# Optimization experiments

Measured on AMD Instinct MI355X. Metric: run time of the kernel, lower is better.

The kernel has to match this reference:

```python
import jax, jax.numpy as jnp
import numpy as np

B, S, L, U, E, V = 32, 64, 64, 512, 256, 32000

def setup_inputs() -> dict:
    key = jax.random.key(0)
    ks = jax.random.split(key, 12)
    sc = lambda *d: 0.02
    return {
        "target": jax.random.randint(ks[0], (B, S), 0, V),
        "encoder_outputs": jax.random.normal(ks[1], (B, L, U), jnp.float32),
        "enc_h0": jax.random.normal(ks[2], (B, U), jnp.float32),
        "enc_c0": jax.random.normal(ks[3], (B, U), jnp.float32),
        "emb": jax.random.normal(ks[4], (V, E), jnp.float32) * 0.02,
        "W_x": jax.random.normal(ks[5], (E, 4 * U), jnp.float32) * 0.02,
        "W_h": jax.random.normal(ks[6], (U, 4 * U), jnp.float32) * 0.02,
        "b_lstm": jnp.zeros((4 * U,), jnp.float32),
        "Wa": jax.random.normal(ks[7], (U, U), jnp.float32) * 0.02,
        "W_fc": jax.random.normal(ks[8], (2 * U, V), jnp.float32) * 0.02,
        "b_fc": jnp.zeros((V,), jnp.float32),
    }

def reference(target, encoder_outputs, enc_h0, enc_c0, emb, W_x, W_h, b_lstm, Wa, W_fc, b_fc):
    # Teacher forcing (teach_forcing_ran=1): input at step t is target[:, t-1],
    # producing outputs for t = 1 .. seq_maxlen-1.
    x_seq = emb[target[:, : S - 1]]                      # [B, S-1, E]
    x_seq = jnp.transpose(x_seq, (1, 0, 2))              # [S-1, B, E]
    enc_proj = jnp.einsum('blu,uv->blv', encoder_outputs, Wa)  # Luong 'general' projection

    def step(carry, x_t):
        h, c = carry
        z = x_t @ W_x + h @ W_h + b_lstm                 # [B, 4U]
        i, f, g, o = jnp.split(z, 4, axis=-1)            # keras gate order i,f,c,o
        i = jax.nn.sigmoid(i); f = jax.nn.sigmoid(f)
        g = jnp.tanh(g);       o = jax.nn.sigmoid(o)
        c = f * c + i * g
        h = o * jnp.tanh(c)
        score = jnp.einsum('bu,blu->bl', h, enc_proj)    # [B, L]
        attn = jax.nn.softmax(score, axis=-1)
        ctx = jnp.einsum('bl,blu->bu', attn, encoder_outputs)
        logits = jnp.tanh(jnp.concatenate([ctx, h], axis=-1) @ W_fc + b_fc)
        out_t = jax.nn.log_softmax(logits, axis=-1)      # [B, V]
        return (h, c), out_t

    (_, _), outs = jax.lax.scan(step, (enc_h0, enc_c0), x_seq)
    return jnp.transpose(outs, (1, 0, 2))                # [B, S-1, V]
```

## Files before the change

### kernel.cpp

```cpp
#include <hip/hip_runtime.h>
#include <stdint.h>

#define B_   32
#define T_   63
#define U_   512
#define E_   256
#define V_   32000
#define L_   64
#define FU_  2048
#define KFC_ 1024
#define MROW_ 2016

#define NFCX_ 250
#define NFCY_ 16
#define CCNT_BASE 1024
#define AFC_FLAG_U32 (2016 * 512)

typedef float f32x4 __attribute__((ext_vector_type(4)));
typedef float f32x2 __attribute__((ext_vector_type(2)));
typedef __bf16 bf16x8 __attribute__((ext_vector_type(8)));

__device__ __forceinline__ unsigned short f2bf(float f) {
  union { float f; unsigned u; } v; v.f = f;
  unsigned u = v.u;
  u += 0x7FFFu + ((u >> 16) & 1u);
  return (unsigned short)(u >> 16);
}
__device__ __forceinline__ float bf2f(unsigned short h) {
  union { unsigned u; float f; } v; v.u = ((unsigned)h) << 16;
  return v.f;
}
__device__ __forceinline__ float fast_sigmoid(float x) {
  return 1.f / (1.f + __expf(-x));
}
__device__ __forceinline__ float fast_tanh(float x) {
  float e = __expf(2.f * x);
  return 1.f - 2.f / (e + 1.f);
}

__global__ __launch_bounds__(256) void k_prep(const int* __restrict__ target,
    const float* __restrict__ emb, const float* __restrict__ W_x,
    const float* __restrict__ b_lstm, const float* __restrict__ enc_out,
    const float* __restrict__ Wa, const float* __restrict__ W_h,
    unsigned short* __restrict__ fragWh, unsigned short* __restrict__ Zx,
    float* __restrict__ enc_proj, unsigned short* __restrict__ encT,
    unsigned int* __restrict__ hcnt, float* __restrict__ row_sums,
    unsigned int* __restrict__ AfcFlags) {
  __shared__ __align__(16) char smem[32768];
  const int bx = blockIdx.x;
  const int tid = threadIdx.x;

  if (bx < 512) {
    int idx = bx * 256 + tid;
    int lane = idx & 63;
    int kc   = (idx >> 6) & 15;
    int ct   = idx >> 10;
    int quad = lane >> 4, l15 = lane & 15;
    int col = ct * 16 + l15;
    unsigned short* dst = fragWh + (size_t)idx * 8;
#pragma unroll
    for (int j = 0; j < 8; ++j) {
      int k = kc * 32 + quad * 8 + j;
      dst[j] = f2bf(W_h[(size_t)k * FU_ + col]);
    }
  } else if (bx < 1016) {
    float* x_lds = (float*)smem;
    int r = bx - 512;
    int t = r % 63, cc = r / 63;
    for (int i = tid; i < B_ * E_; i += 256) {
      int b = i >> 8, e = i & 255;
      x_lds[i] = emb[(size_t)target[b * 64 + t] * E_ + e];
    }
    __syncthreads();
    int col = cc * 256 + tid;
    float acc[B_];
#pragma unroll
    for (int b = 0; b < B_; ++b) acc[b] = 0.f;
    for (int e4 = 0; e4 < E_ / 4; ++e4) {
      float w0 = W_x[(size_t)(4 * e4 + 0) * FU_ + col];
      float w1 = W_x[(size_t)(4 * e4 + 1) * FU_ + col];
      float w2 = W_x[(size_t)(4 * e4 + 2) * FU_ + col];
      float w3 = W_x[(size_t)(4 * e4 + 3) * FU_ + col];
#pragma unroll
      for (int b = 0; b < B_; ++b) {
        f32x4 xv = *(const f32x4*)&x_lds[b * E_ + 4 * e4];
        acc[b] += xv[0] * w0 + xv[1] * w1 + xv[2] * w2 + xv[3] * w3;
      }
    }
    float bias = b_lstm[col];
#pragma unroll
    for (int b = 0; b < B_; ++b)
      Zx[((size_t)(t * B_ + b)) * FU_ + col] = f2bf(acc[b] + bias);
  } else if (bx < 1272) {
    float* e_lds = (float*)smem;
    int r = bx - 1016;
    int rc = r & 127, cc = r >> 7;
    int row0 = rc * 16;
    for (int i = tid; i < 16 * U_; i += 256)
      e_lds[i] = enc_out[(size_t)(row0 + (i >> 9)) * U_ + (i & 511)];
    __syncthreads();
    int col = cc * 256 + tid;
    float acc[16];
#pragma unroll
    for (int q = 0; q < 16; ++q) acc[q] = 0.f;
    for (int k4 = 0; k4 < U_ / 4; ++k4) {
      float w0 = Wa[(size_t)(4 * k4 + 0) * U_ + col];
      float w1 = Wa[(size_t)(4 * k4 + 1) * U_ + col];
      float w2 = Wa[(size_t)(4 * k4 + 2) * U_ + col];
      float w3 = Wa[(size_t)(4 * k4 + 3) * U_ + col];
#pragma unroll
      for (int q = 0; q < 16; ++q) {
        f32x4 xv = *(const f32x4*)&e_lds[q * U_ + 4 * k4];
        acc[q] += xv[0] * w0 + xv[1] * w1 + xv[2] * w2 + xv[3] * w3;
      }
    }
#pragma unroll
    for (int q = 0; q < 16; ++q)
      enc_proj[(size_t)(row0 + q) * U_ + col] = acc[q];
  } else if (bx < 1528) {
    float (*tile)[65] = (float(*)[65])smem;
    int r = bx - 1272;
    int b = r & 31, uc = r >> 5;
#pragma unroll
    for (int i = 0; i < 16; ++i) {
      int idx = i * 256 + tid;
      int l = idx >> 6, u = idx & 63;
      tile[l][u] = enc_out[((size_t)b * L_ + l) * U_ + uc * 64 + u];
    }
    __syncthreads();
#pragma unroll
    for (int i = 0; i < 16; ++i) {
      int idx = i * 256 + tid;
      int u = idx >> 6, l = idx & 63;
      encT[((size_t)b * U_ + uc * 64 + u) * L_ + l] = f2bf(tile[l][u]);
    }
  } else {
    int i = (bx - 1528) * 256 + tid;
    hcnt[i] = 0u;
    if (i < MROW_) row_sums[i] = 0.f;
    AfcFlags[i * 4 + 0] = 0u;
    AfcFlags[i * 4 + 1] = 0u;
    AfcFlags[i * 4 + 2] = 0u;
    AfcFlags[i * 4 + 3] = 0u;
  }
}

__global__ __launch_bounds__(256, 1) void k_rec(const float* __restrict__ enc_h0,
    const float* __restrict__ enc_c0,
    const float* __restrict__ enc_proj, const unsigned short* __restrict__ Zx,
    const unsigned short* __restrict__ fragWh, const unsigned short* __restrict__ encT,
    unsigned int* hseq32,
    unsigned short* __restrict__ Afc,
    unsigned int* hcnt,
    unsigned short* __restrict__ WfcT, const float* __restrict__ b_fc,
    float* __restrict__ out, float* __restrict__ row_sums,
    const float* __restrict__ W_fc) {
  __shared__ __align__(16) char smem[44160];

  const int tid = threadIdx.x;
  unsigned long long* hseq64 = (unsigned long long*)hseq32;
  unsigned int* AfcFlags = (unsigned int*)Afc + AFC_FLAG_U32;

  if (blockIdx.x < 32) {
    unsigned short* h_lds = (unsigned short*)smem;
    float* z_lds = (float*)(smem + 33280);
    float* c_lds = (float*)(smem + 41984);

    const int g = blockIdx.x;
    const int w = tid >> 6;
    const int lane = tid & 63;
    const int quad = lane >> 4;
    const int l15 = lane & 15;
    const int b = tid >> 3;
    const int j = tid & 7;

    const unsigned short* bbase = fragWh + ((size_t)(w * 32 + g) * 16) * 64 * 8;
    bf16x8 bfr[16];
#pragma unroll
    for (int kc = 0; kc < 16; ++kc)
      bfr[kc] = *(const bf16x8*)(bbase + (size_t)(kc * 64 + lane) * 8);

    __builtin_amdgcn_s_setprio(1);

    {
      int u = g * 16 + 2 * j;
      float h0a = enc_h0[(size_t)b * U_ + u];
      float h0b = enc_h0[(size_t)b * U_ + u + 1];
      unsigned pack = (unsigned)f2bf(h0a) | ((unsigned)f2bf(h0b) << 16);
      __hip_atomic_store(&hseq32[b * 256 + g * 8 + j], pack,
                         __ATOMIC_RELAXED, __HIP_MEMORY_SCOPE_AGENT);
      c_lds[b * 17 + 2 * j]     = enc_c0[(size_t)b * U_ + u];
      c_lds[b * 17 + 2 * j + 1] = enc_c0[(size_t)b * U_ + u + 1];
    }
    __syncthreads();
    if (tid == 0)
      __hip_atomic_fetch_add(&hcnt[0], 1u, __ATOMIC_RELAXED, __HIP_MEMORY_SCOPE_AGENT);

    for (int t = 0; t < T_; ++t) {
      const unsigned short* zxbase = Zx + ((size_t)(t * B_ + b)) * FU_ + g * 16 + 2 * j;
      unsigned zxp0 = *(const unsigned*)(zxbase + 0 * U_);
      unsigned zxp1 = *(const unsigned*)(zxbase + 1 * U_);
      unsigned zxp2 = *(const unsigned*)(zxbase + 2 * U_);
      unsigned zxp3 = *(const unsigned*)(zxbase + 3 * U_);

      if (tid == 0) {
        while (__hip_atomic_load(&hcnt[t * 16], __ATOMIC_RELAXED,
                                 __HIP_MEMORY_SCOPE_AGENT) < 32u)
          __builtin_amdgcn_s_sleep(1);
      }
      __syncthreads();

      const unsigned long long* hp = hseq64 + (size_t)t * (B_ * U_ / 4);
      unsigned long long hv[16];
#pragma unroll
      for (int i = 0; i < 16; ++i) {
        hv[i] = __hip_atomic_load(&hp[i * 256 + tid], __ATOMIC_RELAXED,
                                  __HIP_MEMORY_SCOPE_AGENT);
      }
#pragma unroll
      for (int i = 0; i < 16; ++i) {
        int idx = i * 256 + tid;
        int hb = idx >> 7, u0 = (idx & 127) * 4;
        *(unsigned long long*)&h_lds[hb * 520 + u0] = hv[i];
      }
      __syncthreads();

      f32x4 acc0 = {0.f, 0.f, 0.f, 0.f}, acc1 = {0.f, 0.f, 0.f, 0.f};
#pragma unroll
      for (int kc = 0; kc < 16; ++kc) {
        bf16x8 a0 = *(const bf16x8*)&h_lds[l15 * 520 + kc * 32 + quad * 8];
        bf16x8 a1 = *(const bf16x8*)&h_lds[(16 + l15) * 520 + kc * 32 + quad * 8];
        acc0 = __builtin_amdgcn_mfma_f32_16x16x32_bf16(a0, bfr[kc], acc0, 0, 0, 0);
        acc1 = __builtin_amdgcn_mfma_f32_16x16x32_bf16(a1, bfr[kc], acc1, 0, 0, 0);
      }
#pragma unroll
      for (int r = 0; r < 4; ++r) {
        z_lds[(quad * 4 + r) * 68 + w * 16 + l15] = acc0[r];
        z_lds[(16 + quad * 4 + r) * 68 + w * 16 + l15] = acc1[r];
      }
      __syncthreads();

      {
        int up0 = 2 * j, up1 = 2 * j + 1;
        float zi0 = z_lds[b * 68 + 0 + up0] + bf2f((unsigned short)(zxp0 & 0xFFFFu));
        float zi1 = z_lds[b * 68 + 0 + up1] + bf2f((unsigned short)(zxp0 >> 16));
        float zf0 = z_lds[b * 68 + 16 + up0] + bf2f((unsigned short)(zxp1 & 0xFFFFu));
        float zf1 = z_lds[b * 68 + 16 + up1] + bf2f((unsigned short)(zxp1 >> 16));
        float zg0 = z_lds[b * 68 + 32 + up0] + bf2f((unsigned short)(zxp2 & 0xFFFFu));
        float zg1 = z_lds[b * 68 + 32 + up1] + bf2f((unsigned short)(zxp2 >> 16));
        float zo0 = z_lds[b * 68 + 48 + up0] + bf2f((unsigned short)(zxp3 & 0xFFFFu));
        float zo1 = z_lds[b * 68 + 48 + up1] + bf2f((unsigned short)(zxp3 >> 16));
        float i0 = fast_sigmoid(zi0), i1 = fast_sigmoid(zi1);
        float f0 = fast_sigmoid(zf0), f1 = fast_sigmoid(zf1);
        float g0 = fast_tanh(zg0),    g1 = fast_tanh(zg1);
        float o0 = fast_sigmoid(zo0), o1 = fast_sigmoid(zo1);
        float c0 = f0 * c_lds[b * 17 + up0] + i0 * g0;
        float c1 = f1 * c_lds[b * 17 + up1] + i1 * g1;
        c_lds[b * 17 + up0] = c0;
        c_lds[b * 17 + up1] = c1;
        float h0 = o0 * fast_tanh(c0);
        float h1 = o1 * fast_tanh(c1);
        unsigned pack = (unsigned)f2bf(h0) | ((unsigned)f2bf(h1) << 16);
        __hip_atomic_store(&hseq32[(size_t)(t + 1) * (B_ * U_ / 2) + b * 256 + g * 8 + j],
                           pack, __ATOMIC_RELAXED, __HIP_MEMORY_SCOPE_AGENT);
        __hip_atomic_store(
            (unsigned*)&Afc[(size_t)(t * B_ + b) * KFC_ + U_ + g * 16 + 2 * j],
            pack, __ATOMIC_RELAXED, __HIP_MEMORY_SCOPE_AGENT);
      }
      __syncthreads();
      if (tid == 0)
        __hip_atomic_fetch_add(&hcnt[(t + 1) * 16], 1u,
                               __ATOMIC_RELAXED, __HIP_MEMORY_SCOPE_AGENT);
    }
  } else if (blockIdx.x < 64) {
    float* h_sh    = (float*)smem;
    float* sc_part = (float*)(smem + 2048);
    float* probs   = (float*)(smem + 3072);

    __builtin_amdgcn_s_setprio(1);
    const int b = blockIdx.x - 32;
    for (int t = 0; t < T_; ++t) {
      if (tid == 0) {
        while (__hip_atomic_load(&hcnt[(t + 1) * 16], __ATOMIC_RELAXED,
                                 __HIP_MEMORY_SCOPE_AGENT) < 32u)
          __builtin_amdgcn_s_sleep(2);
      }
      __syncthreads();
      if (tid < 128) {
        unsigned long long v = __hip_atomic_load(
            &hseq64[(size_t)(t + 1) * (B_ * U_ / 4) + b * 128 + tid],
            __ATOMIC_RELAXED, __HIP_MEMORY_SCOPE_AGENT);
        int u0 = tid * 4;
        h_sh[u0 + 0] = bf2f((unsigned short)(v & 0xFFFFu));
        h_sh[u0 + 1] = bf2f((unsigned short)((v >> 16) & 0xFFFFu));
        h_sh[u0 + 2] = bf2f((unsigned short)((v >> 32) & 0xFFFFu));
        h_sh[u0 + 3] = bf2f((unsigned short)((v >> 48) & 0xFFFFu));
      }
      __syncthreads();
      {
        int l = tid & 63, part = tid >> 6;
        const float* ep = enc_proj + ((size_t)(b * L_ + l)) * U_ + part * 128;
        const float* hs = h_sh + part * 128;
        float s = 0.f;
#pragma unroll 8
        for (int u = 0; u < 128; u += 4) {
          f32x4 e = *(const f32x4*)(ep + u);
          s += hs[u] * e[0] + hs[u + 1] * e[1] + hs[u + 2] * e[2] + hs[u + 3] * e[3];
        }
        sc_part[part * L_ + l] = s;
      }
      __syncthreads();
      if (tid < 64) {
        float s = sc_part[tid] + sc_part[64 + tid] + sc_part[128 + tid] + sc_part[192 + tid];
        float m = s;
#pragma unroll
        for (int off = 32; off >= 1; off >>= 1) m = fmaxf(m, __shfl_xor(m, off));
        float e = __expf(s - m);
        float sum = e;
#pragma unroll
        for (int off = 32; off >= 1; off >>= 1) sum += __shfl_xor(sum, off);
        probs[tid] = e / sum;
      }
      __syncthreads();
      {
        int u0 = 2 * tid;
        const unsigned short* ep0 = encT + ((size_t)b * U_ + u0) * L_;
        float c0 = 0.f, c1 = 0.f;
#pragma unroll
        for (int l8 = 0; l8 < 8; ++l8) {
          bf16x8 e0 = *(const bf16x8*)(ep0 + l8 * 8);
          bf16x8 e1 = *(const bf16x8*)(ep0 + L_ + l8 * 8);
#pragma unroll
          for (int q = 0; q < 8; ++q) {
            float p = probs[l8 * 8 + q];
            c0 += p * (float)e0[q];
            c1 += p * (float)e1[q];
          }
        }
        unsigned pack = (unsigned)f2bf(c0) | ((unsigned)f2bf(c1) << 16);
        __hip_atomic_store((unsigned*)&Afc[(size_t)(t * B_ + b) * KFC_ + u0], pack,
                           __ATOMIC_RELAXED, __HIP_MEMORY_SCOPE_AGENT);
      }
      __syncthreads();
      if (tid == 0)
        __hip_atomic_fetch_add(&hcnt[CCNT_BASE + t * 16], 1u,
                               __ATOMIC_RELAXED, __HIP_MEMORY_SCOPE_AGENT);
    }
  } else {
    unsigned short* At = (unsigned short*)smem;
    unsigned short* Bt = (unsigned short*)(smem + 8192);
    float* rs = (float*)(smem + 16384);

    const int idx = blockIdx.x - 64;
    const int cx = idx % NFCX_, ry = idx / NFCX_;
    int t_hi = 4 * ry + 3; if (t_hi > T_ - 1) t_hi = T_ - 1;

    if (ry == 0) {
      float* tile = (float*)smem;
      const int n0 = cx * 128;
      for (int kt2 = 0; kt2 < 32; ++kt2) {
        int k0 = kt2 * 32;
#pragma unroll
        for (int it = 0; it < 4; ++it) {
          int lin = it * 256 + tid;
          int k = lin >> 5, nq = lin & 31;
          f32x4 v = *(const f32x4*)(W_fc + (size_t)(k0 + k) * V_ + n0 + nq * 4);
          *(f32x4*)&tile[k * 132 + nq * 4] = v;
        }
        __syncthreads();
#pragma unroll
        for (int it = 0; it < 4; ++it) {
          int lin = it * 256 + tid;
          int n = lin >> 3, kq = lin & 7;
          float a0 = tile[(kq * 4 + 0) * 132 + n];
          float a1 = tile[(kq * 4 + 1) * 132 + n];
          float a2 = tile[(kq * 4 + 2) * 132 + n];
          float a3 = tile[(kq * 4 + 3) * 132 + n];
          unsigned long long pk =
              (unsigned long long)((unsigned)f2bf(a0) | ((unsigned)f2bf(a1) << 16)) |
              ((unsigned long long)((unsigned)f2bf(a2) | ((unsigned)f2bf(a3) << 16)) << 32);
          __hip_atomic_store(
              (unsigned long long*)&WfcT[(size_t)(n0 + n) * KFC_ + k0 + kq * 4], pk,
              __ATOMIC_RELAXED, __HIP_MEMORY_SCOPE_AGENT);
        }
        __syncthreads();
      }
      if (tid == 0)
        __hip_atomic_store(&AfcFlags[cx * 16], 1u,
                           __ATOMIC_RELAXED, __HIP_MEMORY_SCOPE_AGENT);
    }

    if (tid == 0) {
      if (ry != 0) {
        while (__hip_atomic_load(&AfcFlags[cx * 16], __ATOMIC_RELAXED,
                                 __HIP_MEMORY_SCOPE_AGENT) == 0u)
          __builtin_amdgcn_s_sleep(16);
      }
      while (__hip_atomic_load(&hcnt[CCNT_BASE + t_hi * 16], __ATOMIC_RELAXED,
                               __HIP_MEMORY_SCOPE_AGENT) < 32u)
        __builtin_amdgcn_s_sleep(32);
    }
    __syncthreads();

    const int w = tid >> 6, lane = tid & 63, quad = lane >> 4, l15 = lane & 15;
    const int row0 = ry * 128, col0 = cx * 128;
    const int mh = (w >> 1) * 64, nh = (w & 1) * 64;

    f32x4 acc[4][4];
#pragma unroll
    for (int i = 0; i < 4; ++i)
#pragma unroll
      for (int j = 0; j < 4; ++j) { f32x4 z = {0.f, 0.f, 0.f, 0.f}; acc[i][j] = z; }

    for (int kt = 0; kt < KFC_ / 32; ++kt) {
      int k0 = kt * 32;
#pragma unroll
      for (int i = 0; i < 2; ++i) {
        int lin = i * 256 + tid;
        int r = lin >> 2, s = lin & 3;
        int gseg = (s - (r >> 1)) & 3;
        f32x4 va = *(const f32x4*)(Afc + ((size_t)(row0 + r)) * KFC_ + k0 + gseg * 8);
        *(f32x4*)&At[r * 32 + s * 8] = va;
        f32x4 vb = *(const f32x4*)(WfcT + ((size_t)(col0 + r)) * KFC_ + k0 + gseg * 8);
        *(f32x4*)&Bt[r * 32 + s * 8] = vb;
      }
      __syncthreads();
      bf16x8 a[4], b[4];
#pragma unroll
      for (int i = 0; i < 4; ++i) {
        int m = mh + i * 16 + l15;
        a[i] = *(const bf16x8*)&At[m * 32 + (((quad + (m >> 1)) & 3) * 8)];
        int n = nh + i * 16 + l15;
        b[i] = *(const bf16x8*)&Bt[n * 32 + (((quad + (n >> 1)) & 3) * 8)];
      }
#pragma unroll
      for (int i = 0; i < 4; ++i)
#pragma unroll
        for (int j = 0; j < 4; ++j)
          acc[i][j] = __builtin_amdgcn_mfma_f32_16x16x32_bf16(a[i], b[j], acc[i][j], 0, 0, 0);
      __syncthreads();
    }

    if (tid < 128) rs[tid] = 0.f;
    __syncthreads();
    float bv[4];
#pragma unroll
    for (int j = 0; j < 4; ++j) bv[j] = b_fc[col0 + nh + j * 16 + l15];
    float rp[4][4];
#pragma unroll
    for (int i = 0; i < 4; ++i)
#pragma unroll
      for (int r = 0; r < 4; ++r) rp[i][r] = 0.f;
#pragma unroll
    for (int i = 0; i < 4; ++i) {
#pragma unroll
      for (int j = 0; j < 4; ++j) {
        int cg = col0 + nh + j * 16 + l15;
#pragma unroll
        for (int r = 0; r < 4; ++r) {
          float val = fast_tanh(acc[i][j][r] + bv[j]);
          int rg = row0 + mh + i * 16 + quad * 4 + r;
          if (rg < MROW_) {
            int b = rg & 31, t = rg >> 5;
            out[((size_t)(b * T_ + t)) * V_ + cg] = val;
          }
          rp[i][r] += __expf(val);
        }
      }
    }
#pragma unroll
    for (int i = 0; i < 4; ++i)
#pragma unroll
      for (int r = 0; r < 4; ++r) {
        float v = rp[i][r];
        v += __shfl_xor(v, 1); v += __shfl_xor(v, 2);
        v += __shfl_xor(v, 4); v += __shfl_xor(v, 8);
        if (l15 == 0) atomicAdd(&rs[mh + i * 16 + quad * 4 + r], v);
      }
    __syncthreads();
    if (tid < 128) {
      int rg = row0 + tid;
      if (rg < MROW_) atomicAdd(&row_sums[rg], rs[tid]);
    }
  }
}

__global__ __launch_bounds__(256) void k_lsm(float* __restrict__ out,
                                             const float* __restrict__ row_sums, int n4) {
  int i = blockIdx.x * 256 + threadIdx.x;
  if (i >= n4) return;
  f32x4* o4 = (f32x4*)out;
  f32x4 v = o4[i];
  int r = i / 8000;
  int b = r / 63, t = r - b * 63;
  float ls = __logf(row_sums[t * 32 + b]);
  v[0] -= ls; v[1] -= ls; v[2] -= ls; v[3] -= ls;
  o4[i] = v;
}

extern "C" void kernel_launch(void* const* d_in, const int* in_sizes, int n_in,
                              void* d_out, int out_size, void* d_ws, size_t ws_size,
                              hipStream_t stream) {
  const int*   target  = (const int*)d_in[0];
  const float* enc_out = (const float*)d_in[1];
  const float* enc_h0  = (const float*)d_in[2];
  const float* enc_c0  = (const float*)d_in[3];
  const float* emb     = (const float*)d_in[4];
  const float* W_x     = (const float*)d_in[5];
  const float* W_h     = (const float*)d_in[6];
  const float* b_lstm  = (const float*)d_in[7];
  const float* Wa      = (const float*)d_in[8];
  const float* W_fc    = (const float*)d_in[9];
  const float* b_fc    = (const float*)d_in[10];
  float* out = (float*)d_out;
  char* ws = (char*)d_ws;

  unsigned int*   hcnt     = (unsigned int*)(ws + 0);
  float*          row_sums = (float*)(ws + 8192);
  unsigned short* fragWh   = (unsigned short*)(ws + 16384);
  unsigned int*   hseq32   = (unsigned int*)(ws + 2113536);
  unsigned short* Zx       = (unsigned short*)(ws + 4210688);
  float*          enc_proj = (float*)(ws + 12468224);
  unsigned short* Afc      = (unsigned short*)(ws + 16662528);
  unsigned short* encT     = (unsigned short*)(ws + 20856832);
  unsigned short* WfcT     = (unsigned short*)(ws + 22953984);

  unsigned int* AfcFlags = (unsigned int*)(ws + 16662528 + (size_t)AFC_FLAG_U32 * 4);

  k_prep <<<dim3(1536),         dim3(256), 0, stream>>>(target, emb, W_x, b_lstm,
                                                        enc_out, Wa, W_h,
                                                        fragWh, Zx, enc_proj, encT,
                                                        hcnt, row_sums, AfcFlags);
  k_rec  <<<dim3(64 + NFCX_ * NFCY_), dim3(256), 0, stream>>>(enc_h0, enc_c0,
                                                        enc_proj, Zx, fragWh, encT,
                                                        hseq32, Afc, hcnt,
                                                        WfcT, b_fc, out, row_sums,
                                                        W_fc);
  k_lsm  <<<dim3(63000),        dim3(256), 0, stream>>>(out, row_sums, 16128000);
}
```

Baseline: 1.064 ms.

## Use 512-thread blocks: halve recurrent blocks, per-block flags, pack two FC tiles

The persistent kernel now runs 512-thread blocks. The LSTM recurrence is split over 16 blocks, each computing 32 hidden units with eight waves and two weight fragments held in registers. The single atomic counter per step is replaced by per-block flags, which 64 threads poll with a wave vote. Attention blocks use eight partial score slices, and each FC block processes two 128x128 tiles in separate LDS halves. The aim is to cut barrier and counter contention on the serial recurrence and the block count, at the cost of more registers per thread and possible occupancy or co-residency risks for the spin-waiting blocks.

```diff
diff --git a/kernel.cpp b/kernel.cpp
--- a/kernel.cpp
+++ b/kernel.cpp
@@ -17,7 +17,6 @@
 #define AFC_FLAG_U32 (2016 * 512)
 
 typedef float f32x4 __attribute__((ext_vector_type(4)));
-typedef float f32x2 __attribute__((ext_vector_type(2)));
 typedef __bf16 bf16x8 __attribute__((ext_vector_type(8)));
 
 __device__ __forceinline__ unsigned short f2bf(float f) {
@@ -145,7 +144,7 @@
   }
 }
 
-__global__ __launch_bounds__(256, 1) void k_rec(const float* __restrict__ enc_h0,
+__global__ __launch_bounds__(512, 2) void k_rec(const float* __restrict__ enc_h0,
     const float* __restrict__ enc_c0,
     const float* __restrict__ enc_proj, const unsigned short* __restrict__ Zx,
     const unsigned short* __restrict__ fragWh, const unsigned short* __restrict__ encT,
@@ -155,71 +154,79 @@
     unsigned short* __restrict__ WfcT, const float* __restrict__ b_fc,
     float* __restrict__ out, float* __restrict__ row_sums,
     const float* __restrict__ W_fc) {
-  __shared__ __align__(16) char smem[44160];
+  __shared__ __align__(16) char smem[54528];
 
   const int tid = threadIdx.x;
   unsigned long long* hseq64 = (unsigned long long*)hseq32;
   unsigned int* AfcFlags = (unsigned int*)Afc + AFC_FLAG_U32;
 
-  if (blockIdx.x < 32) {
+  if (blockIdx.x < 16) {
     unsigned short* h_lds = (unsigned short*)smem;
     float* z_lds = (float*)(smem + 33280);
-    float* c_lds = (float*)(smem + 41984);
-
-    const int g = blockIdx.x;
-    const int w = tid >> 6;
+    float* c_lds = (float*)(smem + 50176);
+
+    const int p = blockIdx.x;
+    const int ww = tid >> 6;
+    const int w = ww & 3;
+    const int hf = ww >> 2;
     const int lane = tid & 63;
     const int quad = lane >> 4;
     const int l15 = lane & 15;
-    const int b = tid >> 3;
-    const int j = tid & 7;
-
-    const unsigned short* bbase = fragWh + ((size_t)(w * 32 + g) * 16) * 64 * 8;
-    bf16x8 bfr[16];
-#pragma unroll
-    for (int kc = 0; kc < 16; ++kc)
-      bfr[kc] = *(const bf16x8*)(bbase + (size_t)(kc * 64 + lane) * 8);
+    const int b = tid >> 4;
+    const int j = tid & 15;
+
+    bf16x8 bfr[2][16];
+#pragma unroll
+    for (int s = 0; s < 2; ++s) {
+      const unsigned short* bbase = fragWh + ((size_t)(w * 32 + 2 * p + s) * 16) * 512;
+#pragma unroll
+      for (int kc = 0; kc < 16; ++kc)
+        bfr[s][kc] = *(const bf16x8*)(bbase + (size_t)(kc * 64 + lane) * 8);
+    }
 
     __builtin_amdgcn_s_setprio(1);
 
     {
-      int u = g * 16 + 2 * j;
+      int u = 32 * p + 2 * j;
       float h0a = enc_h0[(size_t)b * U_ + u];
       float h0b = enc_h0[(size_t)b * U_ + u + 1];
       unsigned pack = (unsigned)f2bf(h0a) | ((unsigned)f2bf(h0b) << 16);
-      __hip_atomic_store(&hseq32[b * 256 + g * 8 + j], pack,
+      __hip_atomic_store(&hseq32[b * 256 + 16 * p + j], pack,
                          __ATOMIC_RELAXED, __HIP_MEMORY_SCOPE_AGENT);
-      c_lds[b * 17 + 2 * j]     = enc_c0[(size_t)b * U_ + u];
-      c_lds[b * 17 + 2 * j + 1] = enc_c0[(size_t)b * U_ + u + 1];
+      c_lds[b * 34 + 2 * j]     = enc_c0[(size_t)b * U_ + u];
+      c_lds[b * 34 + 2 * j + 1] = enc_c0[(size_t)b * U_ + u + 1];
     }
     __syncthreads();
     if (tid == 0)
-      __hip_atomic_fetch_add(&hcnt[0], 1u, __ATOMIC_RELAXED, __HIP_MEMORY_SCOPE_AGENT);
+      __hip_atomic_store(&hcnt[p], 1u, __ATOMIC_RELAXED, __HIP_MEMORY_SCOPE_AGENT);
 
     for (int t = 0; t < T_; ++t) {
-      const unsigned short* zxbase = Zx + ((size_t)(t * B_ + b)) * FU_ + g * 16 + 2 * j;
+      const unsigned short* zxbase = Zx + ((size_t)(t * B_ + b)) * FU_ + 32 * p + 2 * j;
       unsigned zxp0 = *(const unsigned*)(zxbase + 0 * U_);
       unsigned zxp1 = *(const unsigned*)(zxbase + 1 * U_);
       unsigned zxp2 = *(const unsigned*)(zxbase + 2 * U_);
       unsigned zxp3 = *(const unsigned*)(zxbase + 3 * U_);
 
-      if (tid == 0) {
-        while (__hip_atomic_load(&hcnt[t * 16], __ATOMIC_RELAXED,
-                                 __HIP_MEMORY_SCOPE_AGENT) < 32u)
+      if (tid < 64) {
+        int pl = tid & 15;
+        while (true) {
+          unsigned v = __hip_atomic_load(&hcnt[t * 16 + pl], __ATOMIC_RELAXED,
+                                         __HIP_MEMORY_SCOPE_AGENT);
+          if (__all(v != 0u)) break;
           __builtin_amdgcn_s_sleep(1);
-      }
-      __syncthreads();
-
-      const unsigned long long* hp = hseq64 + (size_t)t * (B_ * U_ / 4);
-      unsigned long long hv[16];
-#pragma unroll
-      for (int i = 0; i < 16; ++i) {
-        hv[i] = __hip_atomic_load(&hp[i * 256 + tid], __ATOMIC_RELAXED,
+        }
+      }
+      __syncthreads();
+
+      const unsigned long long* hp = hseq64 + (size_t)t * 4096;
+      unsigned long long hv[8];
+#pragma unroll
+      for (int i = 0; i < 8; ++i)
+        hv[i] = __hip_atomic_load(&hp[i * 512 + tid], __ATOMIC_RELAXED,
                                   __HIP_MEMORY_SCOPE_AGENT);
-      }
-#pragma unroll
-      for (int i = 0; i < 16; ++i) {
-        int idx = i * 256 + tid;
+#pragma unroll
+      for (int i = 0; i < 8; ++i) {
+        int idx = i * 512 + tid;
         int hb = idx >> 7, u0 = (idx & 127) * 4;
         *(unsigned long long*)&h_lds[hb * 520 + u0] = hv[i];
       }
@@ -228,67 +235,71 @@
       f32x4 acc0 = {0.f, 0.f, 0.f, 0.f}, acc1 = {0.f, 0.f, 0.f, 0.f};
 #pragma unroll
       for (int kc = 0; kc < 16; ++kc) {
-        bf16x8 a0 = *(const bf16x8*)&h_lds[l15 * 520 + kc * 32 + quad * 8];
-        bf16x8 a1 = *(const bf16x8*)&h_lds[(16 + l15) * 520 + kc * 32 + quad * 8];
-        acc0 = __builtin_amdgcn_mfma_f32_16x16x32_bf16(a0, bfr[kc], acc0, 0, 0, 0);
-        acc1 = __builtin_amdgcn_mfma_f32_16x16x32_bf16(a1, bfr[kc], acc1, 0, 0, 0);
+        bf16x8 av = *(const bf16x8*)&h_lds[(hf * 16 + l15) * 520 + kc * 32 + quad * 8];
+        acc0 = __builtin_amdgcn_mfma_f32_16x16x32_bf16(av, bfr[0][kc], acc0, 0, 0, 0);
+        acc1 = __builtin_amdgcn_mfma_f32_16x16x32_bf16(av, bfr[1][kc], acc1, 0, 0, 0);
       }
 #pragma unroll
       for (int r = 0; r < 4; ++r) {
-        z_lds[(quad * 4 + r) * 68 + w * 16 + l15] = acc0[r];
-        z_lds[(16 + quad * 4 + r) * 68 + w * 16 + l15] = acc1[r];
+        z_lds[(hf * 16 + quad * 4 + r) * 132 + w * 32 + l15]      = acc0[r];
+        z_lds[(hf * 16 + quad * 4 + r) * 132 + w * 32 + 16 + l15] = acc1[r];
       }
       __syncthreads();
 
       {
         int up0 = 2 * j, up1 = 2 * j + 1;
-        float zi0 = z_lds[b * 68 + 0 + up0] + bf2f((unsigned short)(zxp0 & 0xFFFFu));
-        float zi1 = z_lds[b * 68 + 0 + up1] + bf2f((unsigned short)(zxp0 >> 16));
-        float zf0 = z_lds[b * 68 + 16 + up0] + bf2f((unsigned short)(zxp1 & 0xFFFFu));
-        float zf1 = z_lds[b * 68 + 16 + up1] + bf2f((unsigned short)(zxp1 >> 16));
-        float zg0 = z_lds[b * 68 + 32 + up0] + bf2f((unsigned short)(zxp2 & 0xFFFFu));
-        float zg1 = z_lds[b * 68 + 32 + up1] + bf2f((unsigned short)(zxp2 >> 16));
-        float zo0 = z_lds[b * 68 + 48 + up0] + bf2f((unsigned short)(zxp3 & 0xFFFFu));
-        float zo1 = z_lds[b * 68 + 48 + up1] + bf2f((unsigned short)(zxp3 >> 16));
+        const float* zb = z_lds + b * 132;
+        float zi0 = zb[ 0 + up0] + bf2f((unsigned short)(zxp0 & 0xFFFFu));
+        float zi1 = zb[ 0 + up1] + bf2f((unsigned short)(zxp0 >> 16));
+        float zf0 = zb[32 + up0] + bf2f((unsigned short)(zxp1 & 0xFFFFu));
+        float zf1 = zb[32 + up1] + bf2f((unsigned short)(zxp1 >> 16));
+        float zg0 = zb[64 + up0] + bf2f((unsigned short)(zxp2 & 0xFFFFu));
+        float zg1 = zb[64 + up1] + bf2f((unsigned short)(zxp2 >> 16));
+        float zo0 = zb[96 + up0] + bf2f((unsigned short)(zxp3 & 0xFFFFu));
+        float zo1 = zb[96 + up1] + bf2f((unsigned short)(zxp3 >> 16));
         float i0 = fast_sigmoid(zi0), i1 = fast_sigmoid(zi1);
         float f0 = fast_sigmoid(zf0), f1 = fast_sigmoid(zf1);
         float g0 = fast_tanh(zg0),    g1 = fast_tanh(zg1);
         float o0 = fast_sigmoid(zo0), o1 = fast_sigmoid(zo1);
-        float c0 = f0 * c_lds[b * 17 + up0] + i0 * g0;
-        float c1 = f1 * c_lds[b * 17 + up1] + i1 * g1;
-        c_lds[b * 17 + up0] = c0;
-        c_lds[b * 17 + up1] = c1;
+        float c0 = f0 * c_lds[b * 34 + up0] + i0 * g0;
+        float c1 = f1 * c_lds[b * 34 + up1] + i1 * g1;
+        c_lds[b * 34 + up0] = c0;
+        c_lds[b * 34 + up1] = c1;
         float h0 = o0 * fast_tanh(c0);
         float h1 = o1 * fast_tanh(c1);
         unsigned pack = (unsigned)f2bf(h0) | ((unsigned)f2bf(h1) << 16);
-        __hip_atomic_store(&hseq32[(size_t)(t + 1) * (B_ * U_ / 2) + b * 256 + g * 8 + j],
+        __hip_atomic_store(&hseq32[(size_t)(t + 1) * 8192 + b * 256 + 16 * p + j],
                            pack, __ATOMIC_RELAXED, __HIP_MEMORY_SCOPE_AGENT);
         __hip_atomic_store(
-            (unsigned*)&Afc[(size_t)(t * B_ + b) * KFC_ + U_ + g * 16 + 2 * j],
+            (unsigned*)&Afc[(size_t)(t * B_ + b) * KFC_ + U_ + 32 * p + 2 * j],
             pack, __ATOMIC_RELAXED, __HIP_MEMORY_SCOPE_AGENT);
       }
       __syncthreads();
       if (tid == 0)
-        __hip_atomic_fetch_add(&hcnt[(t + 1) * 16], 1u,
-                               __ATOMIC_RELAXED, __HIP_MEMORY_SCOPE_AGENT);
-    }
-  } else if (blockIdx.x < 64) {
+        __hip_atomic_store(&hcnt[(t + 1) * 16 + p], 1u,
+                           __ATOMIC_RELAXED, __HIP_MEMORY_SCOPE_AGENT);
+    }
+  } else if (blockIdx.x < 48) {
     float* h_sh    = (float*)smem;
     float* sc_part = (float*)(smem + 2048);
-    float* probs   = (float*)(smem + 3072);
+    float* probs   = (float*)(smem + 4096);
 
     __builtin_amdgcn_s_setprio(1);
-    const int b = blockIdx.x - 32;
+    const int b = blockIdx.x - 16;
     for (int t = 0; t < T_; ++t) {
-      if (tid == 0) {
-        while (__hip_atomic_load(&hcnt[(t + 1) * 16], __ATOMIC_RELAXED,
-                                 __HIP_MEMORY_SCOPE_AGENT) < 32u)
+      if (tid < 64) {
+        int pl = tid & 15;
+        while (true) {
+          unsigned v = __hip_atomic_load(&hcnt[(t + 1) * 16 + pl], __ATOMIC_RELAXED,
+                                         __HIP_MEMORY_SCOPE_AGENT);
+          if (__all(v != 0u)) break;
           __builtin_amdgcn_s_sleep(2);
+        }
       }
       __syncthreads();
       if (tid < 128) {
         unsigned long long v = __hip_atomic_load(
-            &hseq64[(size_t)(t + 1) * (B_ * U_ / 4) + b * 128 + tid],
+            &hseq64[(size_t)(t + 1) * 4096 + b * 128 + tid],
             __ATOMIC_RELAXED, __HIP_MEMORY_SCOPE_AGENT);
         int u0 = tid * 4;
         h_sh[u0 + 0] = bf2f((unsigned short)(v & 0xFFFFu));
@@ -299,19 +310,21 @@
       __syncthreads();
       {
         int l = tid & 63, part = tid >> 6;
-        const float* ep = enc_proj + ((size_t)(b * L_ + l)) * U_ + part * 128;
-        const float* hs = h_sh + part * 128;
+        const float* ep = enc_proj + ((size_t)(b * L_ + l)) * U_ + part * 64;
+        const float* hs = h_sh + part * 64;
         float s = 0.f;
-#pragma unroll 8
-        for (int u = 0; u < 128; u += 4) {
+#pragma unroll
+        for (int u = 0; u < 64; u += 4) {
           f32x4 e = *(const f32x4*)(ep + u);
           s += hs[u] * e[0] + hs[u + 1] * e[1] + hs[u + 2] * e[2] + hs[u + 3] * e[3];
         }
-        sc_part[part * L_ + l] = s;
+        sc_part[part * 64 + l] = s;
       }
       __syncthreads();
       if (tid < 64) {
-        float s = sc_part[tid] + sc_part[64 + tid] + sc_part[128 + tid] + sc_part[192 + tid];
+        float s = 0.f;
+#pragma unroll
+        for (int q = 0; q < 8; ++q) s += sc_part[q * 64 + tid];
         float m = s;
 #pragma unroll
         for (int off = 32; off >= 1; off >>= 1) m = fmaxf(m, __shfl_xor(m, off));
@@ -323,23 +336,21 @@
       }
       __syncthreads();
       {
-        int u0 = 2 * tid;
-        const unsigned short* ep0 = encT + ((size_t)b * U_ + u0) * L_;
-        float c0 = 0.f, c1 = 0.f;
+        int u = tid;
+        const unsigned short* ep0 = encT + ((size_t)b * U_ + u) * L_;
+        float c0 = 0.f;
 #pragma unroll
         for (int l8 = 0; l8 < 8; ++l8) {
           bf16x8 e0 = *(const bf16x8*)(ep0 + l8 * 8);
-          bf16x8 e1 = *(const bf16x8*)(ep0 + L_ + l8 * 8);
-#pragma unroll
-          for (int q = 0; q < 8; ++q) {
-            float p = probs[l8 * 8 + q];
-            c0 += p * (float)e0[q];
-            c1 += p * (float)e1[q];
-          }
-        }
-        unsigned pack = (unsigned)f2bf(c0) | ((unsigned)f2bf(c1) << 16);
-        __hip_atomic_store((unsigned*)&Afc[(size_t)(t * B_ + b) * KFC_ + u0], pack,
-                           __ATOMIC_RELAXED, __HIP_MEMORY_SCOPE_AGENT);
+#pragma unroll
+          for (int q = 0; q < 8; ++q) c0 += probs[l8 * 8 + q] * (float)e0[q];
+        }
+        float c1 = __shfl_xor(c0, 1);
+        if ((tid & 1) == 0) {
+          unsigned pack = (unsigned)f2bf(c0) | ((unsigned)f2bf(c1) << 16);
+          __hip_atomic_store((unsigned*)&Afc[(size_t)(t * B_ + b) * KFC_ + u], pack,
+                             __ATOMIC_RELAXED, __HIP_MEMORY_SCOPE_AGENT);
+        }
       }
       __syncthreads();
       if (tid == 0)
@@ -347,22 +358,26 @@
                                __ATOMIC_RELAXED, __HIP_MEMORY_SCOPE_AGENT);
     }
   } else {
-    unsigned short* At = (unsigned short*)smem;
-    unsigned short* Bt = (unsigned short*)(smem + 8192);
-    float* rs = (float*)(smem + 16384);
-
-    const int idx = blockIdx.x - 64;
-    const int cx = idx % NFCX_, ry = idx / NFCX_;
+    const int t2 = tid & 255;
+    const int half = tid >> 8;
+    char* sm = smem + half * 17408;
+    unsigned short* At = (unsigned short*)sm;
+    unsigned short* Bt = (unsigned short*)(sm + 8192);
+    float* rs = (float*)(sm + 16384);
+
+    const int fcid = blockIdx.x - 48;
+    const int ti = fcid * 2 + half;
+    const int cx = ti % NFCX_, ry = ti / NFCX_;
     int t_hi = 4 * ry + 3; if (t_hi > T_ - 1) t_hi = T_ - 1;
 
-    if (ry == 0) {
-      float* tile = (float*)smem;
+    if (fcid < 125) {
+      float* tile = (float*)sm;
       const int n0 = cx * 128;
       for (int kt2 = 0; kt2 < 32; ++kt2) {
         int k0 = kt2 * 32;
 #pragma unroll
         for (int it = 0; it < 4; ++it) {
-          int lin = it * 256 + tid;
+          int lin = it * 256 + t2;
           int k = lin >> 5, nq = lin & 31;
           f32x4 v = *(const f32x4*)(W_fc + (size_t)(k0 + k) * V_ + n0 + nq * 4);
           *(f32x4*)&tile[k * 132 + nq * 4] = v;
@@ -370,7 +385,7 @@
         __syncthreads();
 #pragma unroll
         for (int it = 0; it < 4; ++it) {
-          int lin = it * 256 + tid;
+          int lin = it * 256 + t2;
           int n = lin >> 3, kq = lin & 7;
           float a0 = tile[(kq * 4 + 0) * 132 + n];
           float a1 = tile[(kq * 4 + 1) * 132 + n];
@@ -385,12 +400,12 @@
         }
         __syncthreads();
       }
-      if (tid == 0)
+      if (t2 == 0)
         __hip_atomic_store(&AfcFlags[cx * 16], 1u,
                            __ATOMIC_RELAXED, __HIP_MEMORY_SCOPE_AGENT);
     }
 
-    if (tid == 0) {
+    if (t2 == 0) {
       if (ry != 0) {
         while (__hip_atomic_load(&AfcFlags[cx * 16], __ATOMIC_RELAXED,
                                  __HIP_MEMORY_SCOPE_AGENT) == 0u)
@@ -402,7 +417,7 @@
     }
     __syncthreads();
 
-    const int w = tid >> 6, lane = tid & 63, quad = lane >> 4, l15 = lane & 15;
+    const int w = t2 >> 6, lane = t2 & 63, quad = lane >> 4, l15 = lane & 15;
     const int row0 = ry * 128, col0 = cx * 128;
     const int mh = (w >> 1) * 64, nh = (w & 1) * 64;
 
@@ -410,13 +425,13 @@
 #pragma unroll
     for (int i = 0; i < 4; ++i)
 #pragma unroll
-      for (int j = 0; j < 4; ++j) { f32x4 z = {0.f, 0.f, 0.f, 0.f}; acc[i][j] = z; }
+      for (int jj = 0; jj < 4; ++jj) { f32x4 z = {0.f, 0.f, 0.f, 0.f}; acc[i][jj] = z; }
 
     for (int kt = 0; kt < KFC_ / 32; ++kt) {
       int k0 = kt * 32;
 #pragma unroll
       for (int i = 0; i < 2; ++i) {
-        int lin = i * 256 + tid;
+        int lin = i * 256 + t2;
         int r = lin >> 2, s = lin & 3;
         int gseg = (s - (r >> 1)) & 3;
         f32x4 va = *(const f32x4*)(Afc + ((size_t)(row0 + r)) * KFC_ + k0 + gseg * 8);
@@ -436,16 +451,16 @@
 #pragma unroll
       for (int i = 0; i < 4; ++i)
 #pragma unroll
-        for (int j = 0; j < 4; ++j)
-          acc[i][j] = __builtin_amdgcn_mfma_f32_16x16x32_bf16(a[i], b[j], acc[i][j], 0, 0, 0);
-      __syncthreads();
-    }
-
-    if (tid < 128) rs[tid] = 0.f;
+        for (int jj = 0; jj < 4; ++jj)
+          acc[i][jj] = __builtin_amdgcn_mfma_f32_16x16x32_bf16(a[i], b[jj], acc[i][jj], 0, 0, 0);
+      __syncthreads();
+    }
+
+    if (t2 < 128) rs[t2] = 0.f;
     __syncthreads();
     float bv[4];
 #pragma unroll
-    for (int j = 0; j < 4; ++j) bv[j] = b_fc[col0 + nh + j * 16 + l15];
+    for (int jj = 0; jj < 4; ++jj) bv[jj] = b_fc[col0 + nh + jj * 16 + l15];
     float rp[4][4];
 #pragma unroll
     for (int i = 0; i < 4; ++i)
@@ -454,11 +469,11 @@
 #pragma unroll
     for (int i = 0; i < 4; ++i) {
 #pragma unroll
-      for (int j = 0; j < 4; ++j) {
-        int cg = col0 + nh + j * 16 + l15;
+      for (int jj = 0; jj < 4; ++jj) {
+        int cg = col0 + nh + jj * 16 + l15;
 #pragma unroll
         for (int r = 0; r < 4; ++r) {
-          float val = fast_tanh(acc[i][j][r] + bv[j]);
+          float val = fast_tanh(acc[i][jj][r] + bv[jj]);
           int rg = row0 + mh + i * 16 + quad * 4 + r;
           if (rg < MROW_) {
             int b = rg & 31, t = rg >> 5;
@@ -478,9 +493,9 @@
         if (l15 == 0) atomicAdd(&rs[mh + i * 16 + quad * 4 + r], v);
       }
     __syncthreads();
-    if (tid < 128) {
-      int rg = row0 + tid;
-      if (rg < MROW_) atomicAdd(&row_sums[rg], rs[tid]);
+    if (t2 < 128) {
+      int rg = row0 + t2;
+      if (rg < MROW_) atomicAdd(&row_sums[rg], rs[t2]);
     }
   }
 }
@@ -527,14 +542,14 @@
 
   unsigned int* AfcFlags = (unsigned int*)(ws + 16662528 + (size_t)AFC_FLAG_U32 * 4);
 
-  k_prep <<<dim3(1536),         dim3(256), 0, stream>>>(target, emb, W_x, b_lstm,
-                                                        enc_out, Wa, W_h,
-                                                        fragWh, Zx, enc_proj, encT,
-                                                        hcnt, row_sums, AfcFlags);
-  k_rec  <<<dim3(64 + NFCX_ * NFCY_), dim3(256), 0, stream>>>(enc_h0, enc_c0,
-                                                        enc_proj, Zx, fragWh, encT,
-                                                        hseq32, Afc, hcnt,
-                                                        WfcT, b_fc, out, row_sums,
-                                                        W_fc);
-  k_lsm  <<<dim3(63000),        dim3(256), 0, stream>>>(out, row_sums, 16128000);
-}
+  k_prep <<<dim3(1536),  dim3(256), 0, stream>>>(target, emb, W_x, b_lstm,
+                                                 enc_out, Wa, W_h,
+                                                 fragWh, Zx, enc_proj, encT,
+                                                 hcnt, row_sums, AfcFlags);
+  k_rec  <<<dim3(2048),  dim3(512), 0, stream>>>(enc_h0, enc_c0,
+                                                 enc_proj, Zx, fragWh, encT,
+                                                 hseq32, Afc, hcnt,
+                                                 WfcT, b_fc, out, row_sums,
+                                                 W_fc);
+  k_lsm  <<<dim3(63000), dim3(256), 0, stream>>>(out, row_sums, 16128000);
+}
```

Result: faster. 961.1 us (-9.6%).
